# Optimization experiments

Hardware: AMD Instinct MI355X
Metric: run time of the kernel (lower is better)

The kernel has to match this reference:

```python
import jax, jax.numpy as jnp
import numpy as np


def _att(xf, W1, W2):
    # xf: [B, L, dk]; low-rank attention scores, softmax over last dim
    dk = W1.shape[0]
    s1 = xf @ W1                                   # [B, L, 10]
    s2 = jnp.einsum('rk,bjk->brj', W2, xf)         # [B, 10, L]
    scores = jnp.einsum('bir,brj->bij', s1, s2) / jnp.sqrt(jnp.float32(dk))
    return jax.nn.softmax(scores, axis=-1)         # [B, L, L]


def setup_inputs() -> dict:
    B, Ci, Co, N, T = 8, 64, 64, 1000, 24
    ks = jax.random.split(jax.random.key(0), 16)
    f32 = jnp.float32
    return {
        'x': jax.random.normal(ks[0], (B, Ci, N, T), f32),
        'A_adj': jax.random.uniform(ks[1], (N, N), f32),
        'att0_W1': jax.random.normal(ks[2], (N * T, 10), f32) * 0.02,
        'att0_W2': jax.random.normal(ks[3], (10, N * T), f32) * 0.02,
        'gatt_W1': jax.random.normal(ks[4], (Ci * T, 10), f32) * 0.02,
        'gatt_W2': jax.random.normal(ks[5], (10, Ci * T), f32) * 0.02,
        'gcn_W': jax.random.normal(ks[6], (Ci, Co), f32) * 0.05,
        'tatt_W1': jax.random.normal(ks[7], (N * Co, 10), f32) * 0.02,
        'tatt_W2': jax.random.normal(ks[8], (10, N * Co), f32) * 0.02,
        'conv1_w': jax.random.normal(ks[9], (Co, Co, 1, 2), f32) * 0.05,
        'conv1_b': jax.random.normal(ks[10], (Co,), f32) * 0.05,
        'conv2_w': jax.random.normal(ks[11], (Co, Co, 1, 2), f32) * 0.05,
        'conv2_b': jax.random.normal(ks[12], (Co,), f32) * 0.05,
        'res_w': jax.random.normal(ks[13], (Co, Ci, 1, 1), f32) * 0.05,
        'res_b': jax.random.normal(ks[14], (Co,), f32) * 0.05,
        'ln_g': jnp.ones((Co,), f32),
        'ln_b': jnp.zeros((Co,), f32),
    }


def reference(x, A_adj, att0_W1, att0_W2, gatt_W1, gatt_W2, gcn_W,
              tatt_W1, tatt_W2, conv1_w, conv1_b, conv2_w, conv2_b,
              res_w, res_b, ln_g, ln_b):
    B, C, N, T = x.shape
    # ---- block-level channel attention (requires_value=True) ----
    xf = x.reshape(B, C, N * T)
    x1 = (_att(xf, att0_W1, att0_W2) @ xf).reshape(B, C, N, T)
    # ---- GCN block: attention-gated adjacency + graph matmul ----
    xg = jnp.transpose(x1, (0, 2, 1, 3)).reshape(B, N, C * T)
    Ag = _att(xg, gatt_W1, gatt_W2) * A_adj                  # [B, N, N]
    g1 = jnp.einsum('bnm,bcmt->bnct', Ag, x1)                # [B, N, C, T]
    g = jnp.einsum('bnct,co->bont', g1, gcn_W)               # [B, Co, N, T]
    Co = g.shape[1]
    # ---- TCN block: temporal attention + dilated causal convs ----
    xt = jnp.transpose(g, (0, 3, 2, 1)).reshape(B, T, N * Co)
    x2 = (_att(xt, tatt_W1, tatt_W2) @ xt).reshape(B, T, N, Co)
    x2 = jnp.transpose(x2, (0, 3, 2, 1))                     # [B, Co, N, T]
    for w, b, d in ((conv1_w, conv1_b, 1), (conv2_w, conv2_b, 2)):
        y = jax.lax.conv_general_dilated(
            x2, w, (1, 1), [(0, 0), (d, d)], rhs_dilation=(1, d),
            dimension_numbers=('NCHW', 'OIHW', 'NCHW'))
        y = y + b[None, :, None, None]
        x2 = jax.nn.relu(y[..., :-d])                        # trim to T
    # ---- 1x1 residual conv ----
    res = jnp.einsum('bcnt,oc->bont', x, res_w[:, :, 0, 0]) + res_b[None, :, None, None]
    out = jax.nn.relu(x2 + res)
    # ---- LayerNorm over channel dim ----
    o = jnp.transpose(out, (0, 3, 2, 1))                     # [B, T, N, Co]
    mu = o.mean(-1, keepdims=True)
    var = o.var(-1, keepdims=True)
    o = (o - mu) / jnp.sqrt(var + 1e-5) * ln_g + ln_b
    return jnp.transpose(o, (0, 3, 2, 1))                    # [B, Co, N, T]
```

## Files before the change

kernel.cpp:

```cpp
#include <hip/hip_runtime.h>
#include <hip/hip_bf16.h>

typedef unsigned int u32;
typedef unsigned short ushortt;

#define B_  8
#define C_  64
#define N_  1000
#define T_  24
#define R_  10
#define NT_ 24000
#define CT_ 1536
#define NC_ 64000

typedef __attribute__((ext_vector_type(8))) short bf8v;
typedef __attribute__((ext_vector_type(4))) float f4v;

__device__ __forceinline__ ushortt f2b_bits(float f) {
  u32 x = __float_as_uint(f);
  u32 r = (x + 0x7fffu + ((x >> 16) & 1u)) >> 16;
  return (ushortt)r;
}

__device__ __forceinline__ float blockSum256(float v, float* red) {
  red[threadIdx.x] = v; __syncthreads();
  #pragma unroll
  for (int s = 128; s > 0; s >>= 1) {
    if (threadIdx.x < s) red[threadIdx.x] += red[threadIdx.x + s];
    __syncthreads();
  }
  float r = red[0]; __syncthreads();
  return r;
}
__device__ __forceinline__ float blockMax256(float v, float* red) {
  red[threadIdx.x] = v; __syncthreads();
  #pragma unroll
  for (int s = 128; s > 0; s >>= 1) {
    if (threadIdx.x < s) red[threadIdx.x] = fmaxf(red[threadIdx.x], red[threadIdx.x + s]);
    __syncthreads();
  }
  float r = red[0]; __syncthreads();
  return r;
}

__device__ __forceinline__ void ld24f32(const float* p, float* v) {
  #pragma unroll
  for (int t = 0; t < 24; t += 4) {
    float4 f = *(const float4*)&p[t];
    v[t] = f.x; v[t+1] = f.y; v[t+2] = f.z; v[t+3] = f.w;
  }
}

__global__ __launch_bounds__(256) void zerok(float* p, int n) {
  int i = blockIdx.x * 256 + threadIdx.x;
  if (i < n) p[i] = 0.f;
}

__global__ __launch_bounds__(256) void pack_w(
    const float* __restrict__ W1, const float* __restrict__ W2,
    float* __restrict__ Wp, int K) {
  int i = blockIdx.x * 256 + threadIdx.x;
  if (i >= K * 20) return;
  int k = i / 20, r = i - k * 20;
  Wp[i] = (r < 10) ? W1[(size_t)k * 10 + r] : W2[(size_t)(r - 10) * K + k];
}

__global__ __launch_bounds__(256) void pack_tailw(
    const float* __restrict__ c1w, const float* __restrict__ c2w,
    const float* __restrict__ rw, ushortt* __restrict__ Wt) {
  int i = blockIdx.x * 256 + threadIdx.x;
  if (i >= 20480) return;
  float v;
  if (i < 8192) {
    int tap = i >> 12, o = (i >> 6) & 63, c = i & 63;
    v = c1w[(size_t)(o * 64 + c) * 2 + (tap ? 0 : 1)];
  } else if (i < 16384) {
    int j = i - 8192;
    int tap = j >> 12, o = (j >> 6) & 63, c = j & 63;
    v = c2w[(size_t)(o * 64 + c) * 2 + (tap ? 0 : 1)];
  } else {
    int j = i - 16384;
    v = rw[j];
  }
  Wt[i] = f2b_bits(v);
}

__global__ __launch_bounds__(256) void att0_s12(
    const float* __restrict__ x, const float* __restrict__ Wp,
    float* __restrict__ s1, float* __restrict__ s2) {
  __shared__ float red[40 * 257];
  const int row0 = blockIdx.x * 4;
  const int kbase = blockIdx.y * 6000;
  const int tid = threadIdx.x;
  float acc[4][20];
  #pragma unroll
  for (int r = 0; r < 4; ++r)
    #pragma unroll
    for (int j = 0; j < 20; ++j) acc[r][j] = 0.f;
  const float* xb = x + (size_t)row0 * NT_ + kbase;
  const float4* wb4 = (const float4*)Wp + (size_t)kbase * 5;
  #pragma unroll 1
  for (int it = 0; it < 6; ++it) {
    int slot = tid + 256 * it;
    if (slot < 1500) {
      int k = slot * 4;
      float4 xv0 = *(const float4*)&xb[k];
      float4 xv1 = *(const float4*)&xb[NT_ + k];
      float4 xv2 = *(const float4*)&xb[2 * NT_ + k];
      float4 xv3 = *(const float4*)&xb[3 * NT_ + k];
      const float4* w4 = wb4 + (size_t)slot * 20;
      #pragma unroll
      for (int kk = 0; kk < 4; ++kk) {
        float4 wa = w4[kk * 5 + 0], wbv = w4[kk * 5 + 1], wc = w4[kk * 5 + 2],
               wd = w4[kk * 5 + 3], we = w4[kk * 5 + 4];
        float w[20] = {wa.x,wa.y,wa.z,wa.w, wbv.x,wbv.y,wbv.z,wbv.w,
                       wc.x,wc.y,wc.z,wc.w, wd.x,wd.y,wd.z,wd.w,
                       we.x,we.y,we.z,we.w};
        float xs0 = ((const float*)&xv0)[kk];
        float xs1 = ((const float*)&xv1)[kk];
        float xs2 = ((const float*)&xv2)[kk];
        float xs3 = ((const float*)&xv3)[kk];
        #pragma unroll
        for (int j = 0; j < 20; ++j) {
          acc[0][j] += xs0 * w[j];
          acc[1][j] += xs1 * w[j];
          acc[2][j] += xs2 * w[j];
          acc[3][j] += xs3 * w[j];
        }
      }
    }
  }
  #pragma unroll
  for (int half = 0; half < 2; ++half) {
    __syncthreads();
    #pragma unroll
    for (int mm = 0; mm < 40; ++mm) {
      int m = half * 40 + mm;
      red[mm * 257 + tid] = acc[m / 20][m % 20];
    }
    __syncthreads();
    #pragma unroll
    for (int s = 128; s >= 8; s >>= 1) {
      for (int i = tid; i < 40 * s; i += 256) {
        int rr = i / s, col = i - rr * s;
        red[rr * 257 + col] += red[rr * 257 + col + s];
      }
      __syncthreads();
    }
    if (tid < 40) {
      float v = 0.f;
      #pragma unroll
      for (int c = 0; c < 8; ++c) v += red[tid * 257 + c];
      int m = half * 40 + tid;
      int row = row0 + m / 20, j = m % 20;
      if (j < 10) atomicAdd(&s1[row * 10 + j], v);
      else        atomicAdd(&s2[row * 10 + (j - 10)], v);
    }
  }
}

__global__ __launch_bounds__(64) void att0_softmax(
    const float* __restrict__ s1, const float* __restrict__ s2, float* __restrict__ P) {
  int b = blockIdx.x, i = threadIdx.x;
  float r1[R_];
  #pragma unroll
  for (int r = 0; r < R_; ++r) r1[r] = s1[(b * 64 + i) * R_ + r];
  const float scale = rsqrtf(24000.f);
  float row[64]; float m = -1e30f;
  for (int j = 0; j < 64; ++j) {
    const float* s2r = s2 + (size_t)(b * 64 + j) * R_;
    float d = 0.f;
    #pragma unroll
    for (int r = 0; r < R_; ++r) d += r1[r] * s2r[r];
    d *= scale; row[j] = d; m = fmaxf(m, d);
  }
  float s = 0.f;
  for (int j = 0; j < 64; ++j) { float e = __expf(row[j] - m); row[j] = e; s += e; }
  float inv = 1.f / s;
  for (int j = 0; j < 64; ++j) P[((size_t)b * 64 + i) * 64 + j] = row[j] * inv;
}

__global__ __launch_bounds__(256) void att0_apply(
    const float* __restrict__ x, const float* __restrict__ P, float* __restrict__ x1tr) {
  __shared__ float Pss[4160];
  __shared__ float xt[6144];
  int b = blockIdx.y, n0 = blockIdx.x * 4;
  int tid = threadIdx.x;
  for (int i = tid; i < 4096; i += 256)
    Pss[(i >> 6) * 65 + (i & 63)] = P[(size_t)b * 4096 + i];
  {
    const float4* src4 = (const float4*)x;
    float4* dst4 = (float4*)xt;
    for (int i = tid; i < 1536; i += 256) {
      int j = i / 24, q = i - j * 24;
      dst4[i] = src4[(size_t)(b * 64 + j) * 6000 + n0 * 6 + q];
    }
  }
  __syncthreads();
  int ig = tid >> 4, ln = (tid >> 2) & 3, ts = tid & 3;
  float acc[4][6];
  #pragma unroll
  for (int ii = 0; ii < 4; ++ii)
    #pragma unroll
    for (int m = 0; m < 6; ++m) acc[ii][m] = 0.f;
  const float* base = &xt[ln * 24 + ts * 6];
  #pragma unroll 4
  for (int j = 0; j < 64; ++j) {
    float vj[6];
    #pragma unroll
    for (int m = 0; m < 6; ++m) vj[m] = base[j * 96 + m];
    #pragma unroll
    for (int ii = 0; ii < 4; ++ii) {
      float p = Pss[(ig * 4 + ii) * 65 + j];
      #pragma unroll
      for (int m = 0; m < 6; ++m) acc[ii][m] += p * vj[m];
    }
  }
  float* drow = x1tr + ((size_t)b * N_ + n0 + ln) * CT_ + ts * 6;
  #pragma unroll
  for (int ii = 0; ii < 4; ++ii) {
    float* d = drow + (ig * 4 + ii) * 24;
    *(float2*)&d[0] = make_float2(acc[ii][0], acc[ii][1]);
    *(float2*)&d[2] = make_float2(acc[ii][2], acc[ii][3]);
    *(float2*)&d[4] = make_float2(acc[ii][4], acc[ii][5]);
  }
}

__global__ __launch_bounds__(256) void transpose_x1(
    const float* __restrict__ x1tr, ushortt* __restrict__ Xbt) {
  __shared__ float s[64][65];
  int b = blockIdx.z, n0 = blockIdx.y * 64, c0 = blockIdx.x * 64;
  int tid = threadIdx.x;
  int r = tid >> 2, cc = (tid & 3) * 16;
  if (n0 + r < N_) {
    const float* src = x1tr + ((size_t)b * N_ + n0 + r) * CT_ + c0 + cc;
    #pragma unroll
    for (int i = 0; i < 16; i += 4) {
      float4 v = *(const float4*)&src[i];
      s[r][cc + i] = v.x; s[r][cc + i + 1] = v.y;
      s[r][cc + i + 2] = v.z; s[r][cc + i + 3] = v.w;
    }
  } else {
    #pragma unroll
    for (int i = 0; i < 16; ++i) s[r][cc + i] = 0.f;
  }
  __syncthreads();
  ushortt* dst = Xbt + ((size_t)b * CT_ + c0 + r) * 1024 + n0 + cc;
  #pragma unroll
  for (int i = 0; i < 16; ++i) dst[i] = f2b_bits(s[cc + i][r]);
}

__global__ __launch_bounds__(256) void gatt_s12(
    const float* __restrict__ xg, const float* __restrict__ Wp,
    float* __restrict__ s1, float* __restrict__ s2T) {
  __shared__ float xs[6144];
  __shared__ float red[5120];
  int bn0 = blockIdx.x * 4;
  int tid = threadIdx.x;
  {
    const float4* src4 = (const float4*)(xg + (size_t)bn0 * CT_);
    float4* dst4 = (float4*)xs;
    for (int i = tid; i < 1536; i += 256) dst4[i] = src4[i];
  }
  __syncthreads();
  int rid = tid >> 6, ks = tid & 63;
  float a[20];
  #pragma unroll
  for (int r = 0; r < 20; ++r) a[r] = 0.f;
  for (int k = ks; k < CT_; k += 64) {
    float xv = xs[rid * CT_ + k];
    const float4* wp4 = (const float4*)&Wp[(size_t)k * 20];
    float4 wa = wp4[0], wb = wp4[1], wc = wp4[2], wd = wp4[3], we = wp4[4];
    float wv[20] = {wa.x,wa.y,wa.z,wa.w, wb.x,wb.y,wb.z,wb.w, wc.x,wc.y,wc.z,wc.w,
                    wd.x,wd.y,wd.z,wd.w, we.x,we.y,we.z,we.w};
    #pragma unroll
    for (int r = 0; r < 20; ++r) a[r] += xv * wv[r];
  }
  #pragma unroll
  for (int r = 0; r < 20; ++r) red[tid * 20 + r] = a[r];
  __syncthreads();
  if (tid < 80) {
    int rid2 = tid / 20, r = tid % 20;
    float s = 0.f;
    for (int l = 0; l < 64; ++l) s += red[(rid2 * 64 + l) * 20 + r];
    int row = bn0 + rid2;
    int b = row / N_, n = row - b * N_;
    if (r < 10) s1[row * 10 + r] = s;
    else        s2T[((size_t)b * 10 + (r - 10)) * N_ + n] = s;
  }
}

__global__ __launch_bounds__(256) void gatt_scores(
    const float* __restrict__ s1, const float* __restrict__ s2T,
    const float* __restrict__ Aadj, ushortt* __restrict__ Agb) {
  __shared__ float p[N_];
  __shared__ float r1[R_];
  __shared__ float red[256];
  int b = blockIdx.x / N_, n = blockIdx.x % N_;
  if (threadIdx.x < R_) r1[threadIdx.x] = s1[((size_t)b * N_ + n) * R_ + threadIdx.x];
  __syncthreads();
  const float scale = rsqrtf(1536.f);
  const float* s2b = s2T + (size_t)b * 10 * N_;
  float lmax = -1e30f;
  for (int m = threadIdx.x; m < N_; m += 256) {
    float d = 0.f;
    #pragma unroll
    for (int r = 0; r < R_; ++r) d += r1[r] * s2b[r * N_ + m];
    d *= scale; p[m] = d; lmax = fmaxf(lmax, d);
  }
  float gmax = blockMax256(lmax, red);
  float lsum = 0.f;
  for (int m = threadIdx.x; m < N_; m += 256) {
    float e = __expf(p[m] - gmax); p[m] = e; lsum += e;
  }
  float gsum = blockSum256(lsum, red);
  float inv = 1.f / gsum;
  ushortt* agr = Agb + ((size_t)b * 1024 + n) * 1024;
  const float* ar = Aadj + (size_t)n * N_;
  for (int m = threadIdx.x; m < 1024; m += 256) {
    float v = (m < N_) ? p[m] * inv * ar[m] : 0.f;
    agr[m] = f2b_bits(v);
  }
}

__global__ __launch_bounds__(256) void gemm_mfma(
    const ushortt* __restrict__ Agb, const ushortt* __restrict__ Xbt,
    float* __restrict__ g1) {
  __shared__ ushortt As[4096];
  __shared__ ushortt Bs[4096];
  const int b = blockIdx.z;
  const int n0 = blockIdx.x * 128;
  const int m0 = blockIdx.y * 128;
  const ushortt* Ab = Agb + (size_t)b * 1024 * 1024;
  const ushortt* Bb = Xbt + (size_t)b * 1536 * 1024;
  const int tid = threadIdx.x;
  const int wave = tid >> 6, lane = tid & 63;
  const int wr = (wave >> 1) * 64, wc = (wave & 1) * 64;
  const int lrow = lane >> 2;
  const int lcol = (lane & 3) * 8;
  const int q = lane >> 4, l15 = lane & 15;

  f4v acc[4][4];
  #pragma unroll
  for (int i = 0; i < 4; ++i)
    #pragma unroll
    for (int j = 0; j < 4; ++j) acc[i][j] = (f4v){0.f, 0.f, 0.f, 0.f};

  const ushortt* gA = Ab + (size_t)(m0 + wave * 16 + lrow) * 1024 + lcol;
  const ushortt* gB = Bb + (size_t)(n0 + wave * 16 + lrow) * 1024 + lcol;
  ushortt* lA = &As[wave * 16 * 32];
  ushortt* lB = &Bs[wave * 16 * 32];

  for (int k0 = 0; k0 < 1024; k0 += 32) {
    __syncthreads();
    __builtin_amdgcn_global_load_lds(
      (const __attribute__((address_space(1))) void*)(gA + k0),
      (__attribute__((address_space(3))) void*)lA, 16, 0, 0);
    __builtin_amdgcn_global_load_lds(
      (const __attribute__((address_space(1))) void*)(gA + (size_t)64 * 1024 + k0),
      (__attribute__((address_space(3))) void*)(lA + 64 * 32), 16, 0, 0);
    __builtin_amdgcn_global_load_lds(
      (const __attribute__((address_space(1))) void*)(gB + k0),
      (__attribute__((address_space(3))) void*)lB, 16, 0, 0);
    __builtin_amdgcn_global_load_lds(
      (const __attribute__((address_space(1))) void*)(gB + (size_t)64 * 1024 + k0),
      (__attribute__((address_space(3))) void*)(lB + 64 * 32), 16, 0, 0);
    __syncthreads();
    bf8v af[4], bfr[4];
    #pragma unroll
    for (int i = 0; i < 4; ++i)
      af[i] = *(const bf8v*)&As[(wr + i * 16 + l15) * 32 + q * 8];
    #pragma unroll
    for (int j = 0; j < 4; ++j)
      bfr[j] = *(const bf8v*)&Bs[(wc + j * 16 + l15) * 32 + q * 8];
    #pragma unroll
    for (int i = 0; i < 4; ++i)
      #pragma unroll
      for (int j = 0; j < 4; ++j)
        acc[i][j] = __builtin_amdgcn_mfma_f32_16x16x32_bf16(af[i], bfr[j], acc[i][j], 0, 0, 0);
  }
  #pragma unroll
  for (int i = 0; i < 4; ++i) {
    int rbase = m0 + wr + i * 16 + q * 4;
    #pragma unroll
    for (int r = 0; r < 4; ++r) {
      int gm = rbase + r;
      if (gm < N_) {
        float* dst = g1 + ((size_t)b * N_ + gm) * CT_ + n0 + wc + l15;
        #pragma unroll
        for (int j = 0; j < 4; ++j) dst[j * 16] = acc[i][j][r];
      }
    }
  }
}

__global__ __launch_bounds__(256) void gcn_out(
    const float* __restrict__ g1, const float* __restrict__ W, float* __restrict__ g) {
  __shared__ float gs[6160];
  __shared__ float Ws[4096];
  int b = blockIdx.y, n0 = blockIdx.x * 4;
  int tid = threadIdx.x;
  {
    const float4* src4 = (const float4*)g1;
    float4* dst4 = (float4*)gs;
    for (int i = tid; i < 1536; i += 256) {
      int ln = i / 384, q = i - ln * 384;
      dst4[ln * 385 + q] = src4[(size_t)(b * N_ + n0 + ln) * 384 + q];
    }
  }
  for (int i = tid; i < 4096; i += 256) Ws[i] = W[i];
  __syncthreads();
  int og = tid >> 4, ln = (tid >> 2) & 3, ts = tid & 3;
  float acc[4][6];
  #pragma unroll
  for (int oo = 0; oo < 4; ++oo)
    #pragma unroll
    for (int m = 0; m < 6; ++m) acc[oo][m] = 0.f;
  const float* base = &gs[ln * 1540 + ts * 6];
  #pragma unroll 4
  for (int c = 0; c < 64; ++c) {
    float v[6];
    #pragma unroll
    for (int m = 0; m < 6; ++m) v[m] = base[c * 24 + m];
    float4 w4 = *(const float4*)&Ws[c * 64 + og * 4];
    float wv[4] = {w4.x, w4.y, w4.z, w4.w};
    #pragma unroll
    for (int oo = 0; oo < 4; ++oo)
      #pragma unroll
      for (int m = 0; m < 6; ++m) acc[oo][m] += wv[oo] * v[m];
  }
  #pragma unroll
  for (int oo = 0; oo < 4; ++oo) {
    int o = og * 4 + oo;
    float* d = g + (((size_t)(b * C_ + o)) * N_ + n0 + ln) * T_ + ts * 6;
    *(float2*)&d[0] = make_float2(acc[oo][0], acc[oo][1]);
    *(float2*)&d[2] = make_float2(acc[oo][2], acc[oo][3]);
    *(float2*)&d[4] = make_float2(acc[oo][4], acc[oo][5]);
  }
}

__global__ __launch_bounds__(256) void tatt_s12(
    const float* __restrict__ g, const float* __restrict__ Wp,
    float* __restrict__ s1, float* __restrict__ s2) {
  __shared__ float red[40 * 257];
  const int b = blockIdx.z, t0 = blockIdx.y * 4, n0 = blockIdx.x * 20;
  const int tid = threadIdx.x;
  const int o = tid & 63, nl = tid >> 6;
  float acc[4][20];
  #pragma unroll
  for (int tt = 0; tt < 4; ++tt)
    #pragma unroll
    for (int j = 0; j < 20; ++j) acc[tt][j] = 0.f;
  const float* gb = g + (size_t)(b * 64 + o) * NT_ + t0;
  #pragma unroll 1
  for (int it = 0; it < 5; ++it) {
    int n = n0 + it * 4 + nl;
    float4 gv = *(const float4*)&gb[n * 24];
    const float4* w4 = (const float4*)&Wp[(size_t)(n * 64 + o) * 20];
    float4 wa = w4[0], wbv = w4[1], wc = w4[2], wd = w4[3], we = w4[4];
    float w[20] = {wa.x,wa.y,wa.z,wa.w, wbv.x,wbv.y,wbv.z,wbv.w,
                   wc.x,wc.y,wc.z,wc.w, wd.x,wd.y,wd.z,wd.w,
                   we.x,we.y,we.z,we.w};
    float gs[4] = {gv.x, gv.y, gv.z, gv.w};
    #pragma unroll
    for (int tt = 0; tt < 4; ++tt)
      #pragma unroll
      for (int j = 0; j < 20; ++j) acc[tt][j] += gs[tt] * w[j];
  }
  #pragma unroll
  for (int half = 0; half < 2; ++half) {
    __syncthreads();
    #pragma unroll
    for (int mm = 0; mm < 40; ++mm) {
      int m = half * 40 + mm;
      red[mm * 257 + tid] = acc[m / 20][m % 20];
    }
    __syncthreads();
    #pragma unroll
    for (int s = 128; s >= 8; s >>= 1) {
      for (int i = tid; i < 40 * s; i += 256) {
        int rr = i / s, col = i - rr * s;
        red[rr * 257 + col] += red[rr * 257 + col + s];
      }
      __syncthreads();
    }
    if (tid < 40) {
      float v = 0.f;
      #pragma unroll
      for (int c = 0; c < 8; ++c) v += red[tid * 257 + c];
      int m = half * 40 + tid;
      int t = t0 + m / 20, j = m % 20;
      if (j < 10) atomicAdd(&s1[(b * T_ + t) * R_ + j], v);
      else        atomicAdd(&s2[(b * T_ + t) * R_ + (j - 10)], v);
    }
  }
}

__global__ __launch_bounds__(64) void tatt_softmax(
    const float* __restrict__ s1, const float* __restrict__ s2, float* __restrict__ Pt) {
  int b = blockIdx.x, t = threadIdx.x;
  if (t >= T_) return;
  float r1[R_];
  #pragma unroll
  for (int r = 0; r < R_; ++r) r1[r] = s1[(b * T_ + t) * R_ + r];
  const float scale = rsqrtf(64000.f);
  float row[T_]; float m = -1e30f;
  for (int j = 0; j < T_; ++j) {
    const float* s2r = s2 + (b * T_ + j) * R_;
    float d = 0.f;
    #pragma unroll
    for (int r = 0; r < R_; ++r) d += r1[r] * s2r[r];
    d *= scale; row[j] = d; m = fmaxf(m, d);
  }
  float s = 0.f;
  for (int j = 0; j < T_; ++j) { float e = __expf(row[j] - m); row[j] = e; s += e; }
  float inv = 1.f / s;
  for (int j = 0; j < T_; ++j) Pt[(b * T_ + t) * T_ + j] = row[j] * inv;
}

__global__ __launch_bounds__(256) void tatt_apply(
    const float* __restrict__ g, const float* __restrict__ Pt, float* __restrict__ x2) {
  __shared__ float P[576];
  int b = blockIdx.y;
  for (int i = threadIdx.x; i < 576; i += 256) P[i] = Pt[b * 576 + i];
  __syncthreads();
  int row = blockIdx.x * 256 + threadIdx.x;
  const float* gp = g + ((size_t)b * 64000 + row) * T_;
  float gr[T_];
  ld24f32(gp, gr);
  float out[T_];
  #pragma unroll
  for (int t = 0; t < T_; ++t) {
    float a = 0.f;
    const float* Pr = &P[t * T_];
    #pragma unroll
    for (int j = 0; j < T_; ++j) a += Pr[j] * gr[j];
    out[t] = a;
  }
  float* xp = x2 + ((size_t)b * 64000 + row) * T_;
  #pragma unroll
  for (int t = 0; t < T_; t += 4)
    *(float4*)&xp[t] = make_float4(out[t], out[t+1], out[t+2], out[t+3]);
}

#define CSB 1024
__global__ __launch_bounds__(256, 3) void tail_k(
    const float* __restrict__ x2, const float* __restrict__ x,
    const ushortt* __restrict__ Wt,
    const float* __restrict__ c1b, const float* __restrict__ c2b,
    const float* __restrict__ rb,
    const float* __restrict__ lg, const float* __restrict__ lb,
    float* __restrict__ outp) {
  __shared__ ushortt X2c[8192];
  __shared__ ushortt Y1c[8192];
  __shared__ ushortt Xrc[8192];
  __shared__ float mu[96], rs[96];
  ushortt* preS = X2c;
  int b = blockIdx.y, n0 = blockIdx.x * 4;
  int tid = threadIdx.x;
  int wave = tid >> 6, lane = tid & 63;
  int q = lane >> 4, l15 = lane & 15;

  for (int i = tid; i < 6144; i += 256) {
    int c = i / 96, rem = i - c * 96;
    int nl = rem / 24, t = rem - nl * 24;
    int col = nl * 32 + 2 + t;
    size_t gidx = ((size_t)(b * 64 + c) * 1000 + n0 + nl) * 24 + t;
    int li = (c >> 3) * CSB + col * 8 + (c & 7);
    X2c[li] = f2b_bits(x2[gidx]);
    Xrc[li] = f2b_bits(x[gidx]);
  }
  {
    int blk = tid >> 5, gi = tid & 31;
    int nl = gi >> 3, gs = gi & 7;
    int s = (gs < 2) ? gs : (24 + gs);
    int col = nl * 32 + s;
    uint4 z = make_uint4(0, 0, 0, 0);
    *(uint4*)&X2c[blk * CSB + col * 8] = z;
    *(uint4*)&Xrc[blk * CSB + col * 8] = z;
  }
  __syncthreads();

  f4v acc1[2][4];
  #pragma unroll
  for (int ct = 0; ct < 2; ++ct)
    #pragma unroll
    for (int mt = 0; mt < 4; ++mt) acc1[ct][mt] = (f4v){0.f, 0.f, 0.f, 0.f};
  #pragma unroll
  for (int ki = 0; ki < 2; ++ki) {
    bf8v a0[4], a1[4];
    #pragma unroll
    for (int mt = 0; mt < 4; ++mt) {
      a0[mt] = *(const bf8v*)&Wt[(mt * 16 + l15) * 64 + ki * 32 + q * 8];
      a1[mt] = *(const bf8v*)&Wt[4096 + (mt * 16 + l15) * 64 + ki * 32 + q * 8];
    }
    #pragma unroll
    for (int ct = 0; ct < 2; ++ct) {
      int col = wave * 32 + ct * 16 + l15;
      int colp = (col == 0) ? 0 : col - 1;
      bf8v bc = *(const bf8v*)&X2c[(ki * 4 + q) * CSB + col * 8];
      bf8v bp = *(const bf8v*)&X2c[(ki * 4 + q) * CSB + colp * 8];
      #pragma unroll
      for (int mt = 0; mt < 4; ++mt) {
        acc1[ct][mt] = __builtin_amdgcn_mfma_f32_16x16x32_bf16(a0[mt], bc, acc1[ct][mt], 0, 0, 0);
        acc1[ct][mt] = __builtin_amdgcn_mfma_f32_16x16x32_bf16(a1[mt], bp, acc1[ct][mt], 0, 0, 0);
      }
    }
  }
  #pragma unroll
  for (int ct = 0; ct < 2; ++ct) {
    int s = ct * 16 + l15;
    int col = wave * 32 + s;
    bool v = (s >= 2 && s <= 25);
    #pragma unroll
    for (int mt = 0; mt < 4; ++mt) {
      int o0 = mt * 16 + q * 4;
      float4 bb = *(const float4*)&c1b[o0];
      float y0 = v ? fmaxf(acc1[ct][mt][0] + bb.x, 0.f) : 0.f;
      float y1 = v ? fmaxf(acc1[ct][mt][1] + bb.y, 0.f) : 0.f;
      float y2 = v ? fmaxf(acc1[ct][mt][2] + bb.z, 0.f) : 0.f;
      float y3 = v ? fmaxf(acc1[ct][mt][3] + bb.w, 0.f) : 0.f;
      u32 lo = (u32)f2b_bits(y0) | ((u32)f2b_bits(y1) << 16);
      u32 hi = (u32)f2b_bits(y2) | ((u32)f2b_bits(y3) << 16);
      *(uint2*)&Y1c[(o0 >> 3) * CSB + col * 8 + (o0 & 7)] = make_uint2(lo, hi);
    }
  }
  __syncthreads();

  f4v accA[2][4], accR[2][4];
  #pragma unroll
  for (int ct = 0; ct < 2; ++ct)
    #pragma unroll
    for (int mt = 0; mt < 4; ++mt) {
      accA[ct][mt] = (f4v){0.f, 0.f, 0.f, 0.f};
      accR[ct][mt] = (f4v){0.f, 0.f, 0.f, 0.f};
    }
  #pragma unroll
  for (int ki = 0; ki < 2; ++ki) {
    bf8v c0[4], c1t[4], rrf[4];
    #pragma unroll
    for (int mt = 0; mt < 4; ++mt) {
      c0[mt]  = *(const bf8v*)&Wt[8192 + (mt * 16 + l15) * 64 + ki * 32 + q * 8];
      c1t[mt] = *(const bf8v*)&Wt[12288 + (mt * 16 + l15) * 64 + ki * 32 + q * 8];
      rrf[mt] = *(const bf8v*)&Wt[16384 + (mt * 16 + l15) * 64 + ki * 32 + q * 8];
    }
    #pragma unroll
    for (int ct = 0; ct < 2; ++ct) {
      int col = wave * 32 + ct * 16 + l15;
      int colp2 = (col < 2) ? col : col - 2;
      bf8v bc = *(const bf8v*)&Y1c[(ki * 4 + q) * CSB + col * 8];
      bf8v bp = *(const bf8v*)&Y1c[(ki * 4 + q) * CSB + colp2 * 8];
      bf8v bx = *(const bf8v*)&Xrc[(ki * 4 + q) * CSB + col * 8];
      #pragma unroll
      for (int mt = 0; mt < 4; ++mt) {
        accA[ct][mt] = __builtin_amdgcn_mfma_f32_16x16x32_bf16(c0[mt], bc, accA[ct][mt], 0, 0, 0);
        accA[ct][mt] = __builtin_amdgcn_mfma_f32_16x16x32_bf16(c1t[mt], bp, accA[ct][mt], 0, 0, 0);
        accR[ct][mt] = __builtin_amdgcn_mfma_f32_16x16x32_bf16(rrf[mt], bx, accR[ct][mt], 0, 0, 0);
      }
    }
  }
  float pre[2][4][4];
  #pragma unroll
  for (int ct = 0; ct < 2; ++ct) {
    int s = ct * 16 + l15;
    bool v = (s >= 2 && s <= 25);
    int p = wave * 24 + s - 2;
    #pragma unroll
    for (int mt = 0; mt < 4; ++mt) {
      int o0 = mt * 16 + q * 4;
      float4 b2 = *(const float4*)&c2b[o0];
      float4 rbv = *(const float4*)&rb[o0];
      float bb2[4] = {b2.x, b2.y, b2.z, b2.w};
      float brv[4] = {rbv.x, rbv.y, rbv.z, rbv.w};
      #pragma unroll
      for (int r = 0; r < 4; ++r) {
        float a = fmaxf(accA[ct][mt][r] + bb2[r], 0.f) + accR[ct][mt][r] + brv[r];
        pre[ct][mt][r] = fmaxf(a, 0.f);
      }
      if (v) {
        u32 lo = (u32)f2b_bits(pre[ct][mt][0]) | ((u32)f2b_bits(pre[ct][mt][1]) << 16);
        u32 hi = (u32)f2b_bits(pre[ct][mt][2]) | ((u32)f2b_bits(pre[ct][mt][3]) << 16);
        *(uint2*)&preS[p * 68 + o0] = make_uint2(lo, hi);
      }
    }
  }
  __syncthreads();
  if (tid < 96) {
    const ushortt* pr = &preS[tid * 68];
    float sm = 0.f, qq = 0.f;
    #pragma unroll 8
    for (int c = 0; c < 64; c += 2) {
      u32 u = *(const u32*)&pr[c];
      float v0 = __uint_as_float(u << 16);
      float v1 = __uint_as_float(u & 0xffff0000u);
      sm += v0 + v1; qq += v0 * v0 + v1 * v1;
    }
    float m = sm * (1.f / 64.f);
    mu[tid] = m;
    rs[tid] = rsqrtf(qq * (1.f / 64.f) - m * m + 1e-5f);
  }
  __syncthreads();
  #pragma unroll
  for (int ct = 0; ct < 2; ++ct) {
    int s = ct * 16 + l15;
    bool v = (s >= 2 && s <= 25);
    if (!v) continue;
    int p = wave * 24 + s - 2;
    int t = s - 2;
    float m = mu[p], rr = rs[p];
    #pragma unroll
    for (int mt = 0; mt < 4; ++mt) {
      int o0 = mt * 16 + q * 4;
      float4 g4 = *(const float4*)&lg[o0];
      float4 b4 = *(const float4*)&lb[o0];
      float gg[4] = {g4.x, g4.y, g4.z, g4.w};
      float bb[4] = {b4.x, b4.y, b4.z, b4.w};
      #pragma unroll
      for (int r = 0; r < 4; ++r) {
        int o = o0 + r;
        float val = (pre[ct][mt][r] - m) * rr * gg[r] + bb[r];
        outp[((size_t)(b * 64 + o) * 1000 + n0 + wave) * 24 + t] = val;
      }
    }
  }
}

extern "C" void kernel_launch(void* const* d_in, const int* in_sizes, int n_in,
                              void* d_out, int out_size, void* d_ws, size_t ws_size,
                              hipStream_t stream) {
  const float* x     = (const float*)d_in[0];
  const float* Aadj  = (const float*)d_in[1];
  const float* a0W1  = (const float*)d_in[2];
  const float* a0W2  = (const float*)d_in[3];
  const float* gW1   = (const float*)d_in[4];
  const float* gW2   = (const float*)d_in[5];
  const float* gcnW  = (const float*)d_in[6];
  const float* tW1   = (const float*)d_in[7];
  const float* tW2   = (const float*)d_in[8];
  const float* c1w   = (const float*)d_in[9];
  const float* c1b   = (const float*)d_in[10];
  const float* c2w   = (const float*)d_in[11];
  const float* c2b   = (const float*)d_in[12];
  const float* rw    = (const float*)d_in[13];
  const float* rb    = (const float*)d_in[14];
  const float* lng   = (const float*)d_in[15];
  const float* lnb   = (const float*)d_in[16];
  float* out = (float*)d_out;

  float* ws = (float*)d_ws;
  float* R1   = ws;
  float* U    = R1 + 12288000;
  float* D    = U + 12288000;
  float* s1_0 = D + 12288000;
  float* s2_0 = s1_0 + 5120;
  float* P0   = s2_0 + 5120;
  float* s1g  = P0 + 32768;
  float* s2gT = s1g + 80000;
  float* s1t  = s2gT + 80000;
  float* s2t  = s1t + 1920;
  float* Ptb  = s2t + 1920;
  float* Wp0  = Ptb + 4608;
  float* Wgp  = Wp0 + 480000;
  float* Wtp  = Wgp + 30720;
  float* Wtl  = Wtp + 1280000;
  ushortt* Xbt = (ushortt*)U;
  ushortt* Agb = (ushortt*)(U + 6291456);
  ushortt* Wtail = (ushortt*)Wtl;
  float* g = U;
  if (ws_size < (size_t)38876416 * 4) return;

  pack_w<<<1875, 256, 0, stream>>>(a0W1, a0W2, Wp0, 24000);
  pack_w<<<120, 256, 0, stream>>>(gW1, gW2, Wgp, 1536);
  pack_w<<<5000, 256, 0, stream>>>(tW1, tW2, Wtp, 64000);
  pack_tailw<<<80, 256, 0, stream>>>(c1w, c2w, rw, Wtail);
  zerok<<<40, 256, 0, stream>>>(s1_0, 10240);
  att0_s12<<<dim3(128, 4), 256, 0, stream>>>(x, Wp0, s1_0, s2_0);
  att0_softmax<<<8, 64, 0, stream>>>(s1_0, s2_0, P0);
  att0_apply<<<dim3(250, 8), 256, 0, stream>>>(x, P0, R1);
  gatt_s12<<<2000, 256, 0, stream>>>(R1, Wgp, s1g, s2gT);
  transpose_x1<<<dim3(24, 16, 8), 256, 0, stream>>>(R1, Xbt);
  gatt_scores<<<8000, 256, 0, stream>>>(s1g, s2gT, Aadj, Agb);
  gemm_mfma<<<dim3(12, 8, 8), 256, 0, stream>>>(Agb, Xbt, D);
  gcn_out<<<dim3(250, 8), 256, 0, stream>>>(D, gcnW, g);
  zerok<<<15, 256, 0, stream>>>(s1t, 3840);
  tatt_s12<<<dim3(50, 6, 8), 256, 0, stream>>>(g, Wtp, s1t, s2t);
  tatt_softmax<<<8, 32, 0, stream>>>(s1t, s2t, Ptb);
  tatt_apply<<<dim3(250, 8), 256, 0, stream>>>(g, Ptb, R1);
  tail_k<<<dim3(250, 8), 256, 0, stream>>>(R1, x, Wtail, c1b, c2b, rb,
                                           lng, lnb, out);
}
```

Baseline: 569.6 us.

## Store temporal-attention output as bf16 and vectorize tail_k staging loads

tatt_apply now writes its output as packed bf16 instead of fp32, which halves that intermediate's write and read traffic. tail_k reads x2 and x with row-contiguous 16-byte vector loads into a padded row-major shared staging area, then transposes into the k-blocked MFMA layout with zero padding. This replaces scattered scalar global loads plus per-element conversion. It adds an extra shared-memory pass and sync, but tail_k already converted x2 to bf16, so accuracy does not change.

```diff
diff --git a/kernel.cpp b/kernel.cpp
--- a/kernel.cpp
+++ b/kernel.cpp
@@ -20,6 +20,10 @@
   u32 x = __float_as_uint(f);
   u32 r = (x + 0x7fffu + ((x >> 16) & 1u)) >> 16;
   return (ushortt)r;
+}
+
+__device__ __forceinline__ u32 f2b_pair(float a, float b) {
+  return (u32)f2b_bits(a) | ((u32)f2b_bits(b) << 16);
 }
 
 __device__ __forceinline__ float blockSum256(float v, float* red) {
@@ -519,7 +523,7 @@
 }
 
 __global__ __launch_bounds__(256) void tatt_apply(
-    const float* __restrict__ g, const float* __restrict__ Pt, float* __restrict__ x2) {
+    const float* __restrict__ g, const float* __restrict__ Pt, ushortt* __restrict__ x2b) {
   __shared__ float P[576];
   int b = blockIdx.y;
   for (int i = threadIdx.x; i < 576; i += 256) P[i] = Pt[b * 576 + i];
@@ -537,15 +541,19 @@
     for (int j = 0; j < T_; ++j) a += Pr[j] * gr[j];
     out[t] = a;
   }
-  float* xp = x2 + ((size_t)b * 64000 + row) * T_;
-  #pragma unroll
-  for (int t = 0; t < T_; t += 4)
-    *(float4*)&xp[t] = make_float4(out[t], out[t+1], out[t+2], out[t+3]);
+  u32 w[12];
+  #pragma unroll
+  for (int t = 0; t < 24; t += 2) w[t >> 1] = f2b_pair(out[t], out[t + 1]);
+  ushortt* xp = x2b + ((size_t)b * 64000 + row) * 24;
+  *(uint4*)&xp[0]  = make_uint4(w[0], w[1], w[2], w[3]);
+  *(uint4*)&xp[8]  = make_uint4(w[4], w[5], w[6], w[7]);
+  *(uint4*)&xp[16] = make_uint4(w[8], w[9], w[10], w[11]);
 }
 
 #define CSB 1024
+#define RSB 104
 __global__ __launch_bounds__(256, 3) void tail_k(
-    const float* __restrict__ x2, const float* __restrict__ x,
+    const ushortt* __restrict__ x2b, const float* __restrict__ x,
     const ushortt* __restrict__ Wt,
     const float* __restrict__ c1b, const float* __restrict__ c2b,
     const float* __restrict__ rb,
@@ -561,23 +569,65 @@
   int wave = tid >> 6, lane = tid & 63;
   int q = lane >> 4, l15 = lane & 15;
 
-  for (int i = tid; i < 6144; i += 256) {
-    int c = i / 96, rem = i - c * 96;
-    int nl = rem / 24, t = rem - nl * 24;
-    int col = nl * 32 + 2 + t;
-    size_t gidx = ((size_t)(b * 64 + c) * 1000 + n0 + nl) * 24 + t;
-    int li = (c >> 3) * CSB + col * 8 + (c & 7);
-    X2c[li] = f2b_bits(x2[gidx]);
-    Xrc[li] = f2b_bits(x[gidx]);
-  }
+  const int sc = tid >> 2, snl = tid & 3;
+  size_t rowi = ((size_t)(b * 64 + sc) * 1000 + n0 + snl) * 24;
+  uint4 vx2[3];
   {
-    int blk = tid >> 5, gi = tid & 31;
-    int nl = gi >> 3, gs = gi & 7;
-    int s = (gs < 2) ? gs : (24 + gs);
-    int col = nl * 32 + s;
-    uint4 z = make_uint4(0, 0, 0, 0);
-    *(uint4*)&X2c[blk * CSB + col * 8] = z;
-    *(uint4*)&Xrc[blk * CSB + col * 8] = z;
+    const uint4* p = (const uint4*)(x2b + rowi);
+    vx2[0] = p[0]; vx2[1] = p[1]; vx2[2] = p[2];
+  }
+  float4 vx[6];
+  {
+    const float4* p = (const float4*)(x + rowi);
+    #pragma unroll
+    for (int j = 0; j < 6; ++j) vx[j] = p[j];
+  }
+  ushortt* bufA = Y1c;
+  ushortt* bufB = Xrc;
+  {
+    uint4* da = (uint4*)&bufA[sc * RSB + snl * 24];
+    da[0] = vx2[0]; da[1] = vx2[1]; da[2] = vx2[2];
+    u32 w[12];
+    #pragma unroll
+    for (int j = 0; j < 6; ++j) {
+      w[2 * j]     = f2b_pair(vx[j].x, vx[j].y);
+      w[2 * j + 1] = f2b_pair(vx[j].z, vx[j].w);
+    }
+    uint4* db = (uint4*)&bufB[sc * RSB + snl * 24];
+    db[0] = make_uint4(w[0], w[1], w[2], w[3]);
+    db[1] = make_uint4(w[4], w[5], w[6], w[7]);
+    db[2] = make_uint4(w[8], w[9], w[10], w[11]);
+  }
+  __syncthreads();
+  u32 kb[4][4];
+  #pragma unroll
+  for (int rep = 0; rep < 4; ++rep) {
+    int slot = tid + rep * 256;
+    int kblk = slot >> 7, col = slot & 127;
+    int nl2 = col >> 5, s = col & 31;
+    u32 pa[4];
+    if (s >= 2 && s <= 25) {
+      int boff = (kblk * 8) * RSB + nl2 * 24 + (s - 2);
+      #pragma unroll
+      for (int h = 0; h < 4; ++h) {
+        u32 a0 = bufA[boff + (2 * h) * RSB], a1 = bufA[boff + (2 * h + 1) * RSB];
+        pa[h] = a0 | (a1 << 16);
+        u32 b0 = bufB[boff + (2 * h) * RSB], b1 = bufB[boff + (2 * h + 1) * RSB];
+        kb[rep][h] = b0 | (b1 << 16);
+      }
+    } else {
+      #pragma unroll
+      for (int h = 0; h < 4; ++h) { pa[h] = 0u; kb[rep][h] = 0u; }
+    }
+    *(uint4*)&X2c[kblk * CSB + col * 8] = make_uint4(pa[0], pa[1], pa[2], pa[3]);
+  }
+  __syncthreads();
+  #pragma unroll
+  for (int rep = 0; rep < 4; ++rep) {
+    int slot = tid + rep * 256;
+    int kblk = slot >> 7, col = slot & 127;
+    *(uint4*)&Xrc[kblk * CSB + col * 8] =
+        make_uint4(kb[rep][0], kb[rep][1], kb[rep][2], kb[rep][3]);
   }
   __syncthreads();
 
@@ -785,7 +835,7 @@
   zerok<<<15, 256, 0, stream>>>(s1t, 3840);
   tatt_s12<<<dim3(50, 6, 8), 256, 0, stream>>>(g, Wtp, s1t, s2t);
   tatt_softmax<<<8, 32, 0, stream>>>(s1t, s2t, Ptb);
-  tatt_apply<<<dim3(250, 8), 256, 0, stream>>>(g, Ptb, R1);
-  tail_k<<<dim3(250, 8), 256, 0, stream>>>(R1, x, Wtail, c1b, c2b, rb,
-                                           lng, lnb, out);
-}
+  tatt_apply<<<dim3(250, 8), 256, 0, stream>>>(g, Ptb, (ushortt*)R1);
+  tail_k<<<dim3(250, 8), 256, 0, stream>>>((const ushortt*)R1, x, Wtail,
+                                           c1b, c2b, rb, lng, lnb, out);
+}
```

Result: faster. 548.8 us (-3.7%).
